# Kernel tuning notes

Hardware: AMD Instinct MI355X
Metric: run time of the kernel (lower is better)

The kernel has to match this reference:

```python
import jax, jax.numpy as jnp
import numpy as np

N_NODES = 100000
N_EDGES = 600000
NUM_GRAPHS = 512
IN_DIM = 128
HID = 64
HEADS = 2
NEG_SLOPE = 0.2


def gat_layer(h_in, src, dst, W, a_s, a_d, b, n_nodes):
    # W: [F_in, H*C], a_s/a_d: [H, C], b: [H*C]
    H, C = a_s.shape
    h = (h_in @ W).reshape(n_nodes, H, C)            # [N,H,C]
    alpha_src = jnp.einsum('nhc,hc->nh', h, a_s)      # [N,H]
    alpha_dst = jnp.einsum('nhc,hc->nh', h, a_d)      # [N,H]
    e = alpha_src[src] + alpha_dst[dst]               # [E,H]
    e = jnp.where(e >= 0, e, NEG_SLOPE * e)           # leaky_relu
    # segment softmax over destination node
    m = jax.ops.segment_max(e, dst, num_segments=n_nodes)
    m = jnp.where(jnp.isfinite(m), m, 0.0)
    ex = jnp.exp(e - m[dst])                          # [E,H]
    denom = jax.ops.segment_sum(ex, dst, num_segments=n_nodes)
    alpha = ex / jnp.maximum(denom[dst], 1e-16)       # [E,H]
    out = jax.ops.segment_sum(alpha[:, :, None] * h[src], dst, num_segments=n_nodes)
    return out.reshape(n_nodes, H * C) + b


def setup_inputs() -> dict:
    key = jax.random.key(0)
    ks = jax.random.split(key, 16)
    x = jax.random.normal(ks[0], (N_NODES, IN_DIM), dtype=jnp.float32)
    edge_index = jax.random.randint(ks[1], (2, N_EDGES), 0, N_NODES, dtype=jnp.int32)
    batch = jnp.sort(jax.random.randint(ks[2], (N_NODES,), 0, NUM_GRAPHS, dtype=jnp.int32))
    s = lambda *d: 1.0 / np.sqrt(d[0])
    W1 = jax.random.normal(ks[3], (IN_DIM, HEADS * HID), jnp.float32) * s(IN_DIM)
    a_src1 = jax.random.normal(ks[4], (HEADS, HID), jnp.float32) * s(HID)
    a_dst1 = jax.random.normal(ks[5], (HEADS, HID), jnp.float32) * s(HID)
    b1 = jnp.zeros((HEADS * HID,), jnp.float32)
    W2 = jax.random.normal(ks[6], (HEADS * HID, HID), jnp.float32) * s(HEADS * HID)
    a_src2 = jax.random.normal(ks[7], (1, HID), jnp.float32) * s(HID)
    a_dst2 = jax.random.normal(ks[8], (1, HID), jnp.float32) * s(HID)
    b2 = jnp.zeros((HID,), jnp.float32)
    Wf1 = jax.random.normal(ks[9], (2 * HID, HID), jnp.float32) * s(2 * HID)
    bf1 = jnp.zeros((HID,), jnp.float32)
    Wf2 = jax.random.normal(ks[10], (HID, 1), jnp.float32) * s(HID)
    bf2 = jnp.zeros((1,), jnp.float32)
    return dict(x=x, edge_index=edge_index, batch=batch, W1=W1, a_src1=a_src1,
                a_dst1=a_dst1, b1=b1, W2=W2, a_src2=a_src2, a_dst2=a_dst2, b2=b2,
                Wf1=Wf1, bf1=bf1, Wf2=Wf2, bf2=bf2)


def reference(x, edge_index, batch, W1, a_src1, a_dst1, b1, W2, a_src2, a_dst2, b2,
              Wf1, bf1, Wf2, bf2):
    n = x.shape[0]
    loops = jnp.arange(n, dtype=edge_index.dtype)
    src = jnp.concatenate([edge_index[0], loops])
    dst = jnp.concatenate([edge_index[1], loops])
    h = gat_layer(x, src, dst, W1, a_src1, a_dst1, b1, n)
    h = jax.nn.relu(h)
    h = gat_layer(h, src, dst, W2, a_src2, a_dst2, b2, n)  # [N, HID]
    # global mean + max pool per graph
    ones = jnp.ones((n,), h.dtype)
    counts = jax.ops.segment_sum(ones, batch, num_segments=NUM_GRAPHS)  # [G]
    mean = jax.ops.segment_sum(h, batch, num_segments=NUM_GRAPHS) / jnp.maximum(counts, 1.0)[:, None]
    mx = jax.ops.segment_max(h, batch, num_segments=NUM_GRAPHS)
    mx = jnp.where(counts[:, None] > 0, mx, 0.0)
    pooled = jnp.concatenate([mean, mx], axis=1)  # [G, 2*HID]
    out = jax.nn.relu(pooled @ Wf1 + bf1) @ Wf2 + bf2  # [G, 1]
    return out
```

## Files before the change

### kernel.cpp

```cpp
#include <hip/hip_runtime.h>

#define N_NODESC 100000
#define N_EDGESC 600000
#define E_TOTC   700000
#define NUM_GRAPHSC 512
#define NEG_SLOPE 0.2f
#define NEG_INF_ENC 0x007FFFFFu
#define SCAN_NB 128

typedef unsigned short ushort_t;
typedef __attribute__((ext_vector_type(8))) short bf16x8;
typedef __attribute__((ext_vector_type(4))) float f32x4;

__device__ __forceinline__ unsigned enc_f32(float f) {
    unsigned u = __float_as_uint(f);
    return (u & 0x80000000u) ? ~u : (u | 0x80000000u);
}
__device__ __forceinline__ float dec_f32(unsigned u) {
    u = (u & 0x80000000u) ? (u ^ 0x80000000u) : ~u;
    return __uint_as_float(u);
}
__device__ __forceinline__ ushort_t f32_to_bf16(float f) {
    unsigned u = __float_as_uint(f);
    return (ushort_t)((u + 0x7FFFu + ((u >> 16) & 1u)) >> 16);
}
__device__ __forceinline__ float bf16_to_f32(ushort_t h) {
    return __uint_as_float(((unsigned)h) << 16);
}
__device__ __forceinline__ unsigned pack_bf16x2(float a, float b) {
    return (unsigned)f32_to_bf16(a) | ((unsigned)f32_to_bf16(b) << 16);
}

__device__ __forceinline__ void glds16(const void* g, void* l) {
    __builtin_amdgcn_global_load_lds(
        (const __attribute__((address_space(1))) void*)g,
        (__attribute__((address_space(3))) void*)l, 16, 0, 0);
}

__global__ __launch_bounds__(256) void init_all(float* __restrict__ msum,
                                                unsigned* __restrict__ mmax,
                                                float* __restrict__ cnt,
                                                int* __restrict__ deg,
                                                const float* __restrict__ W1,
                                                const float* __restrict__ W2,
                                                ushort_t* __restrict__ wPre1,
                                                ushort_t* __restrict__ wPre2) {
    int i = blockIdx.x * 256 + threadIdx.x;
    if (i < NUM_GRAPHSC * 64) { msum[i] = 0.f; mmax[i] = NEG_INF_ENC; }
    if (i < NUM_GRAPHSC) cnt[i] = 0.f;
    if (i < N_NODESC) deg[i] = 0;
    if (i < 128 * 128) {
        int n = i >> 7, k = i & 127;
        wPre1[n * 128 + k] = f32_to_bf16(W1[k * 128 + n]);
    } else if (i < 128 * 128 + 64 * 128) {
        int j = i - 128 * 128;
        int n = j >> 7, k = j & 127;
        wPre2[n * 128 + k] = f32_to_bf16(W2[k * 64 + n]);
    }
}

__global__ __launch_bounds__(256) void hist_dst(const int* __restrict__ ei,
                                                int* __restrict__ deg) {
    int e = blockIdx.x * blockDim.x + threadIdx.x;
    if (e >= E_TOTC) return;
    int d = (e < N_EDGESC) ? ei[N_EDGESC + e] : e - N_EDGESC;
    atomicAdd(&deg[d], 1);
}

__global__ __launch_bounds__(256) void scan_partial(const int* __restrict__ deg,
                                                    int* __restrict__ bsum, int n) {
    __shared__ int red[256];
    int chunk = (n + SCAN_NB - 1) / SCAN_NB;
    int lo = blockIdx.x * chunk, hi = min(lo + chunk, n);
    int s = 0;
    for (int i = lo + threadIdx.x; i < hi; i += 256) s += deg[i];
    red[threadIdx.x] = s;
    __syncthreads();
    for (int d = 128; d; d >>= 1) {
        if (threadIdx.x < d) red[threadIdx.x] += red[threadIdx.x + d];
        __syncthreads();
    }
    if (threadIdx.x == 0) bsum[blockIdx.x] = red[0];
}

__global__ __launch_bounds__(256) void scan_final(const int* __restrict__ deg,
                                                  const int* __restrict__ bsum,
                                                  int* __restrict__ off, int n) {
    __shared__ int bs[SCAN_NB];
    __shared__ int tile[256];
    __shared__ int carry;
    int t = threadIdx.x;
    if (t < SCAN_NB) bs[t] = bsum[t];
    __syncthreads();
    for (int d = 1; d < SCAN_NB; d <<= 1) {
        int v = (t >= d && t < SCAN_NB) ? bs[t - d] : 0;
        __syncthreads();
        if (t < SCAN_NB) bs[t] += v;
        __syncthreads();
    }
    if (t == 0) carry = blockIdx.x ? bs[blockIdx.x - 1] : 0;
    __syncthreads();
    int chunk = (n + SCAN_NB - 1) / SCAN_NB;
    int lo = blockIdx.x * chunk, hi = min(lo + chunk, n);
    for (int base = lo; base < hi; base += 256) {
        int i = base + t;
        int v = (i < hi) ? deg[i] : 0;
        tile[t] = v;
        __syncthreads();
        for (int d = 1; d < 256; d <<= 1) {
            int u = (t >= d) ? tile[t - d] : 0;
            __syncthreads();
            tile[t] += u;
            __syncthreads();
        }
        if (i < hi) off[i] = carry + tile[t] - v;
        __syncthreads();
        if (t == 0) carry += tile[255];
        __syncthreads();
    }
}

__global__ __launch_bounds__(256) void scatter_csr(const int* __restrict__ ei,
                                                   int* __restrict__ off,
                                                   int* __restrict__ csr) {
    int e = blockIdx.x * blockDim.x + threadIdx.x;
    if (e >= E_TOTC) return;
    int s, d;
    if (e < N_EDGESC) { s = ei[e]; d = ei[N_EDGESC + e]; } else { s = d = e - N_EDGESC; }
    int slot = atomicAdd(&off[d], 1);
    csr[slot] = s;
}

__global__ __launch_bounds__(64) void gemm1_mfma(const float* __restrict__ X,
                                                 const ushort_t* __restrict__ Wp,
                                                 const float* __restrict__ a_s,
                                                 const float* __restrict__ a_d,
                                                 float* __restrict__ as_out,
                                                 float* __restrict__ ad_out,
                                                 ushort_t* __restrict__ Y16, int N) {
    __shared__ float sx[2048];
    int lane = threadIdx.x;
    int quad = lane >> 4, l16 = lane & 15;
    size_t node0 = (size_t)blockIdx.x * 16;

    {
        int rhalf = lane >> 5;
        int cb = (lane & 31) * 16;
#pragma unroll
        for (int c = 0; c < 8; ++c) {
            int rl = 2 * c + rhalf;
            size_t grow = node0 + rl;
            if (grow >= (size_t)N) grow = N - 1;
            int goff = cb ^ ((rl & 15) << 4);
            glds16((const char*)(X + grow * 128) + goff,
                   (char*)sx + c * 1024);
        }
    }
    asm volatile("s_waitcnt vmcnt(0)" ::: "memory");
    __builtin_amdgcn_sched_barrier(0);

    const char* swx = (const char*)sx + l16 * 512;
    int skey = (l16 & 15) << 4;

    f32x4 acc[8];
#pragma unroll
    for (int ct = 0; ct < 8; ++ct) acc[ct] = (f32x4){0.f, 0.f, 0.f, 0.f};

#pragma unroll
    for (int kc = 0; kc < 4; ++kc) {
        int b = kc * 128 + quad * 32;
        float4 xa = *(const float4*)(swx + (b ^ skey));
        float4 xb = *(const float4*)(swx + ((b + 16) ^ skey));
        union { bf16x8 v; unsigned u[4]; } af;
        af.u[0] = pack_bf16x2(xa.x, xa.y);
        af.u[1] = pack_bf16x2(xa.z, xa.w);
        af.u[2] = pack_bf16x2(xb.x, xb.y);
        af.u[3] = pack_bf16x2(xb.z, xb.w);
#pragma unroll
        for (int ct = 0; ct < 8; ++ct) {
            bf16x8 bb = *(const bf16x8*)(Wp + (size_t)(ct * 16 + l16) * 128 + kc * 32 + quad * 8);
            acc[ct] = __builtin_amdgcn_mfma_f32_16x16x32_bf16(af.v, bb, acc[ct], 0, 0, 0);
        }
    }

    unsigned* Yu = (unsigned*)Y16;
    float asv0[4], asv1[4], adv0[4], adv1[4];
#pragma unroll
    for (int ct = 0; ct < 4; ++ct) {
        int c = ct * 16 + l16;
        asv0[ct] = a_s[c]; asv1[ct] = a_s[64 + c];
        adv0[ct] = a_d[c]; adv1[ct] = a_d[64 + c];
    }
#pragma unroll
    for (int r = 0; r < 4; ++r) {
        size_t row = node0 + quad * 4 + r;
        bool ok = row < (size_t)N;
        if (ok) {
#pragma unroll
            for (int ct = 0; ct < 4; ++ct)
                Yu[row * 64 + ct * 16 + l16] = pack_bf16x2(acc[ct][r], acc[ct + 4][r]);
        }
        float ps0 = 0.f, pd0 = 0.f, ps1 = 0.f, pd1 = 0.f;
#pragma unroll
        for (int ct = 0; ct < 4; ++ct) {
            ps0 += acc[ct][r] * asv0[ct];     pd0 += acc[ct][r] * adv0[ct];
            ps1 += acc[ct + 4][r] * asv1[ct]; pd1 += acc[ct + 4][r] * adv1[ct];
        }
#pragma unroll
        for (int sh = 1; sh < 16; sh <<= 1) {
            ps0 += __shfl_xor(ps0, sh); pd0 += __shfl_xor(pd0, sh);
            ps1 += __shfl_xor(ps1, sh); pd1 += __shfl_xor(pd1, sh);
        }
        if (l16 == 0 && ok) {
            *(float2*)(as_out + row * 2) = make_float2(ps0, ps1);
            *(float2*)(ad_out + row * 2) = make_float2(pd0, pd1);
        }
    }
}

template <int H, bool RELU, bool FUSE2>
__global__ __launch_bounds__(256) void gat_gather(const int* __restrict__ off_end,
                                                  const int* __restrict__ deg,
                                                  const int* __restrict__ csr,
                                                  const float* __restrict__ as,
                                                  const float* __restrict__ ad,
                                                  const ushort_t* __restrict__ H16,
                                                  const float* __restrict__ b,
                                                  void* __restrict__ outp,
                                                  const ushort_t* __restrict__ Wp2,
                                                  const float* __restrict__ as2v,
                                                  const float* __restrict__ ad2v,
                                                  float* __restrict__ as2o,
                                                  float* __restrict__ ad2o,
                                                  ushort_t* __restrict__ h2out,
                                                  int N) {
    __shared__ char h1tile[16 * 256];
    __shared__ float aspart[16][4];
    __shared__ float adpart[16][4];
    int lane = threadIdx.x & 63;
    int wave = threadIdx.x >> 6;
    int l = lane & 15;
    int gbase = lane & 48;
    int n = blockIdx.x * 16 + wave * 4 + (lane >> 4);
    if (n >= N) return;
    int dg = deg[n];
    int o = off_end[n] - dg;
    float adv[H];
#pragma unroll
    for (int h = 0; h < H; ++h) adv[h] = ad[n * H + h];

    float acc[H][4], den[H];
#pragma unroll
    for (int h = 0; h < H; ++h) {
        den[h] = 0.f;
#pragma unroll
        for (int q = 0; q < 4; ++q) acc[h][q] = 0.f;
    }

    const unsigned* Hu = (const unsigned*)H16;

    for (int base = 0; base < dg; base += 16) {
        int i = base + l;
        bool valid = i < dg;
        int s = valid ? csr[o + i] : 0;
        float v[H];
        if (H == 2) {
            float2 p = valid ? ((const float2*)as)[s] : make_float2(0.f, 0.f);
            v[0] = p.x + adv[0];
            v[H - 1] = p.y + adv[H - 1];
        } else {
            v[0] = valid ? as[s] + adv[0] : 0.f;
        }
#pragma unroll
        for (int h = 0; h < H; ++h) {
            float e = v[h] >= 0.f ? v[h] : NEG_SLOPE * v[h];
            v[h] = valid ? __expf(e) : 0.f;
            den[h] += v[h];
        }
        int wpk = (H == 2) ? (int)pack_bf16x2(v[0], v[H - 1])
                           : (int)__float_as_uint(v[0]);
        int cnt = min(dg - base, 16);
        int cnt4 = (cnt + 3) & ~3;
        for (int j = 0; j < cnt4; j += 4) {
#pragma unroll
            for (int u = 0; u < 4; ++u) {
                int src = gbase + j + u;
                int sj = __shfl(s, src);
                int wp = __shfl(wpk, src);
                if (H == 2) {
                    float w0 = __uint_as_float(((unsigned)wp) << 16);
                    float w1 = __uint_as_float(((unsigned)wp) & 0xffff0000u);
                    uint4 hu = *(const uint4*)(Hu + (size_t)sj * 64 + l * 4);
                    acc[0][0] += w0 * __uint_as_float(hu.x << 16);
                    acc[H - 1][0] += w1 * __uint_as_float(hu.x & 0xffff0000u);
                    acc[0][1] += w0 * __uint_as_float(hu.y << 16);
                    acc[H - 1][1] += w1 * __uint_as_float(hu.y & 0xffff0000u);
                    acc[0][2] += w0 * __uint_as_float(hu.z << 16);
                    acc[H - 1][2] += w1 * __uint_as_float(hu.z & 0xffff0000u);
                    acc[0][3] += w0 * __uint_as_float(hu.w << 16);
                    acc[H - 1][3] += w1 * __uint_as_float(hu.w & 0xffff0000u);
                } else {
                    float w0 = __uint_as_float((unsigned)wp);
                    uint2 hu = *(const uint2*)((const unsigned*)(H16 + (size_t)sj * 64) + l * 2);
                    acc[0][0] += w0 * __uint_as_float(hu.x << 16);
                    acc[0][1] += w0 * __uint_as_float(hu.x & 0xffff0000u);
                    acc[0][2] += w0 * __uint_as_float(hu.y << 16);
                    acc[0][3] += w0 * __uint_as_float(hu.y & 0xffff0000u);
                }
            }
        }
    }
#pragma unroll
    for (int h = 0; h < H; ++h) {
#pragma unroll
        for (int sh = 8; sh; sh >>= 1) den[h] += __shfl_xor(den[h], sh);
    }
    if (H == 2) {
        float4 b0 = *(const float4*)(b + l * 4);
        float4 b1 = *(const float4*)(b + 64 + l * 4);
        float r0[4], r1[4];
        float id0 = 1.f / fmaxf(den[0], 1e-16f);
        float id1 = 1.f / fmaxf(den[H - 1], 1e-16f);
        r0[0] = acc[0][0] * id0 + b0.x; r0[1] = acc[0][1] * id0 + b0.y;
        r0[2] = acc[0][2] * id0 + b0.z; r0[3] = acc[0][3] * id0 + b0.w;
        r1[0] = acc[H - 1][0] * id1 + b1.x; r1[1] = acc[H - 1][1] * id1 + b1.y;
        r1[2] = acc[H - 1][2] * id1 + b1.z; r1[3] = acc[H - 1][3] * id1 + b1.w;
        if (RELU) {
#pragma unroll
            for (int q = 0; q < 4; ++q) { r0[q] = fmaxf(r0[q], 0.f); r1[q] = fmaxf(r1[q], 0.f); }
        }
        uint2 p0 = make_uint2(pack_bf16x2(r0[0], r0[1]), pack_bf16x2(r0[2], r0[3]));
        uint2 p1 = make_uint2(pack_bf16x2(r1[0], r1[1]), pack_bf16x2(r1[2], r1[3]));
        if (FUSE2) {
            int g = threadIdx.x >> 4;
            int key = (g & 15) << 4;
            *(uint2*)(h1tile + g * 256 + ((l * 8) ^ key)) = p0;
            *(uint2*)(h1tile + g * 256 + ((128 + l * 8) ^ key)) = p1;
        } else {
            ushort_t* outb = (ushort_t*)outp;
            *(uint2*)(outb + (size_t)n * 128 + l * 4) = p0;
            *(uint2*)(outb + (size_t)n * 128 + 64 + l * 4) = p1;
        }
    } else {
        float4 bv = *(const float4*)(b + l * 4);
        float id0 = 1.f / fmaxf(den[0], 1e-16f);
        float4 r;
        r.x = acc[0][0] * id0 + bv.x; r.y = acc[0][1] * id0 + bv.y;
        r.z = acc[0][2] * id0 + bv.z; r.w = acc[0][3] * id0 + bv.w;
        if (RELU) { r.x = fmaxf(r.x, 0.f); r.y = fmaxf(r.y, 0.f);
                    r.z = fmaxf(r.z, 0.f); r.w = fmaxf(r.w, 0.f); }
        *(float4*)((float*)outp + (size_t)n * 64 + l * 4) = r;
    }

    if (FUSE2) {
        __syncthreads();
        int quad = lane >> 4, l16 = lane & 15;
        int skey = (l16 & 15) << 4;
        const char* swx = h1tile + l16 * 256;
        f32x4 acc2 = (f32x4){0.f, 0.f, 0.f, 0.f};
#pragma unroll
        for (int kc = 0; kc < 4; ++kc) {
            int bb_ = kc * 64 + quad * 16;
            bf16x8 a = *(const bf16x8*)(swx + (bb_ ^ skey));
            bf16x8 bb = *(const bf16x8*)(Wp2 + (size_t)(wave * 16 + l16) * 128 + kc * 32 + quad * 8);
            acc2 = __builtin_amdgcn_mfma_f32_16x16x32_bf16(a, bb, acc2, 0, 0, 0);
        }
        float asv = as2v[wave * 16 + l16], adv2 = ad2v[wave * 16 + l16];
        size_t node0 = (size_t)blockIdx.x * 16;
#pragma unroll
        for (int r = 0; r < 4; ++r) {
            size_t row = node0 + quad * 4 + r;
            h2out[row * 64 + wave * 16 + l16] = f32_to_bf16(acc2[r]);
            float ps = acc2[r] * asv, pd = acc2[r] * adv2;
#pragma unroll
            for (int sh = 1; sh < 16; sh <<= 1) {
                ps += __shfl_xor(ps, sh);
                pd += __shfl_xor(pd, sh);
            }
            if (l16 == 0) {
                aspart[quad * 4 + r][wave] = ps;
                adpart[quad * 4 + r][wave] = pd;
            }
        }
        __syncthreads();
        int t = threadIdx.x;
        if (t < 16) {
            as2o[node0 + t] = aspart[t][0] + aspart[t][1] + aspart[t][2] + aspart[t][3];
        } else if (t < 32) {
            int rr = t - 16;
            ad2o[node0 + rr] = adpart[rr][0] + adpart[rr][1] + adpart[rr][2] + adpart[rr][3];
        }
    }
}

__global__ __launch_bounds__(256) void pool_nodes(const float* __restrict__ h2,
                                                  const int* __restrict__ batch,
                                                  float* __restrict__ msum,
                                                  unsigned* __restrict__ mmax,
                                                  float* __restrict__ cnt, int N) {
    int wid = threadIdx.x >> 6, lane = threadIdx.x & 63;
    int n0 = (blockIdx.x * 4 + wid) * 64;
    if (n0 >= N) return;
    int n1 = min(n0 + 64, N);
    int curg = batch[n0];
    float s = 0.f, m = -1e30f;
    int c = 0;
    for (int n = n0; n < n1; ++n) {
        int g = batch[n];
        float v = h2[(size_t)n * 64 + lane];
        if (g != curg) {
            atomicAdd(&msum[curg * 64 + lane], s);
            atomicMax(&mmax[curg * 64 + lane], enc_f32(m));
            if (lane == 0) atomicAdd(&cnt[curg], (float)c);
            s = 0.f; m = -1e30f; c = 0; curg = g;
        }
        s += v;
        m = fmaxf(m, v);
        ++c;
    }
    atomicAdd(&msum[curg * 64 + lane], s);
    atomicMax(&mmax[curg * 64 + lane], enc_f32(m));
    if (lane == 0) atomicAdd(&cnt[curg], (float)c);
}

__global__ __launch_bounds__(64) void mlp_head(const float* __restrict__ msum,
                                               const unsigned* __restrict__ mmax,
                                               const float* __restrict__ cnt,
                                               const float* __restrict__ Wf1,
                                               const float* __restrict__ bf1,
                                               const float* __restrict__ Wf2,
                                               const float* __restrict__ bf2,
                                               float* __restrict__ out) {
    __shared__ float pooled[128];
    int g = blockIdx.x, lane = threadIdx.x;
    float c = cnt[g];
    pooled[lane] = msum[g * 64 + lane] / fmaxf(c, 1.0f);
    pooled[64 + lane] = (c > 0.f) ? dec_f32(mmax[g * 64 + lane]) : 0.f;
    __syncthreads();
    float acc = bf1[lane];
#pragma unroll
    for (int k = 0; k < 128; ++k) acc += pooled[k] * Wf1[k * 64 + lane];
    acc = fmaxf(acc, 0.f);
    float r = acc * Wf2[lane];
#pragma unroll
    for (int off = 32; off; off >>= 1) r += __shfl_xor(r, off);
    if (lane == 0) out[g] = r + bf2[0];
}

extern "C" void kernel_launch(void* const* d_in, const int* in_sizes, int n_in,
                              void* d_out, int out_size, void* d_ws, size_t ws_size,
                              hipStream_t stream) {
    const float* x    = (const float*)d_in[0];
    const int*   ei   = (const int*)d_in[1];
    const int*   batch= (const int*)d_in[2];
    const float* W1   = (const float*)d_in[3];
    const float* as1  = (const float*)d_in[4];
    const float* ad1  = (const float*)d_in[5];
    const float* b1   = (const float*)d_in[6];
    const float* W2   = (const float*)d_in[7];
    const float* as2  = (const float*)d_in[8];
    const float* ad2  = (const float*)d_in[9];
    const float* b2   = (const float*)d_in[10];
    const float* Wf1  = (const float*)d_in[11];
    const float* bf1  = (const float*)d_in[12];
    const float* Wf2  = (const float*)d_in[13];
    const float* bf2  = (const float*)d_in[14];
    float* out = (float*)d_out;

    const size_t N = N_NODESC;
    float* ws = (float*)d_ws;
    ushort_t* h16_1 = (ushort_t*)ws;
    ushort_t* out1b = (ushort_t*)(ws + N * 64);
    ushort_t* h16_2 = (ushort_t*)(ws + N * 128);
    float*    out2  = ws + N * 160;
    float*    small = ws + N * 224;
    float*    as1b = small;
    float*    ad1b = small + 2 * N;
    float*    as2b = small + 4 * N;
    float*    ad2b = small + 5 * N;
    float*    msum = small + 6 * N;
    unsigned* mmax = (unsigned*)(small + 6 * N + 512 * 64);
    float*    cntb = small + 6 * N + 2 * 512 * 64;
    int* ip  = (int*)(small + 6 * N + 2 * 512 * 64 + 512);
    int* deg  = ip;
    int* off  = ip + N;
    int* csr  = ip + 2 * N;
    int* bsum = ip + 2 * N + E_TOTC;
    ushort_t* wPre1 = (ushort_t*)(bsum + SCAN_NB);
    ushort_t* wPre2 = wPre1 + 128 * 128;

    init_all<<<(N_NODESC + 255) / 256, 256, 0, stream>>>(msum, mmax, cntb, deg,
                                                         W1, W2, wPre1, wPre2);

    hist_dst<<<(E_TOTC + 255) / 256, 256, 0, stream>>>(ei, deg);
    scan_partial<<<SCAN_NB, 256, 0, stream>>>(deg, bsum, N);
    scan_final<<<SCAN_NB, 256, 0, stream>>>(deg, bsum, off, N);
    scatter_csr<<<(E_TOTC + 255) / 256, 256, 0, stream>>>(ei, off, csr);

    const int NBLK16 = (N_NODESC + 15) / 16;

    gemm1_mfma<<<NBLK16, 64, 0, stream>>>(x, wPre1, as1, ad1, as1b, ad1b, h16_1, N);
    gat_gather<2, true, true><<<NBLK16, 256, 0, stream>>>(
        off, deg, csr, as1b, ad1b, h16_1, b1, out1b,
        wPre2, as2, ad2, as2b, ad2b, h16_2, N);

    gat_gather<1, false, false><<<NBLK16, 256, 0, stream>>>(
        off, deg, csr, as2b, ad2b, h16_2, b2, out2,
        nullptr, nullptr, nullptr, nullptr, nullptr, nullptr, N);

    pool_nodes<<<(N + 255) / 256, 256, 0, stream>>>(out2, batch, msum, mmax, cntb, N);
    mlp_head<<<NUM_GRAPHSC, 64, 0, stream>>>(msum, mmax, cntb, Wf1, bf1, Wf2, bf2, out);
}
```

Measured before the change: 293.4 us.

## Stage neighbor feature rows into LDS via direct global-to-LDS loads in GAT gather

The gather loop now processes neighbors in batches of 8 instead of 16. Each wave copies the bf16 feature rows of those neighbors straight from global memory into a per-wave LDS buffer with 16-byte direct-to-LDS loads, waits for all of them, then runs the weighted accumulation from LDS. The aim is to issue every neighbor-row load up front and hide gather latency, instead of interleaving dependent global loads with the FMAs. In exchange the kernel gains a large per-block LDS buffer, which can lower occupancy. It also adds a full vmcnt wait every batch and doubles the number of loop iterations for high-degree nodes.

```diff
diff --git a/kernel.cpp b/kernel.cpp
--- a/kernel.cpp
+++ b/kernel.cpp
@@ -234,14 +234,16 @@
                                                   float* __restrict__ ad2o,
                                                   ushort_t* __restrict__ h2out,
                                                   int N) {
+    __shared__ char rbuf[4][(H == 2) ? 8192 : 4096];
     __shared__ char h1tile[16 * 256];
     __shared__ float aspart[16][4];
     __shared__ float adpart[16][4];
     int lane = threadIdx.x & 63;
     int wave = threadIdx.x >> 6;
     int l = lane & 15;
+    int g = lane >> 4;
     int gbase = lane & 48;
-    int n = blockIdx.x * 16 + wave * 4 + (lane >> 4);
+    int n = blockIdx.x * 16 + wave * 4 + g;
     if (n >= N) return;
     int dg = deg[n];
     int o = off_end[n] - dg;
@@ -257,11 +259,9 @@
         for (int q = 0; q < 4; ++q) acc[h][q] = 0.f;
     }
 
-    const unsigned* Hu = (const unsigned*)H16;
-
-    for (int base = 0; base < dg; base += 16) {
+    for (int base = 0; base < dg; base += 8) {
         int i = base + l;
-        bool valid = i < dg;
+        bool valid = (l < 8) && (i < dg);
         int s = valid ? csr[o + i] : 0;
         float v[H];
         if (H == 2) {
@@ -279,18 +279,37 @@
         }
         int wpk = (H == 2) ? (int)pack_bf16x2(v[0], v[H - 1])
                            : (int)__float_as_uint(v[0]);
-        int cnt = min(dg - base, 16);
-        int cnt4 = (cnt + 3) & ~3;
-        for (int j = 0; j < cnt4; j += 4) {
+
+        asm volatile("s_waitcnt lgkmcnt(0)" ::: "memory");
+        if (H == 2) {
+#pragma unroll
+            for (int c = 0; c < 8; ++c) {
+                int sjc = __shfl(s, gbase + c);
+                glds16((const char*)H16 + (size_t)(unsigned)sjc * 256 + l * 16,
+                       &rbuf[wave][c * 1024]);
+            }
+        } else {
+#pragma unroll
+            for (int k = 0; k < 4; ++k) {
+                int sjc = __shfl(s, gbase + 2 * k + (l >> 3));
+                glds16((const char*)H16 + (size_t)(unsigned)sjc * 128 + (l & 7) * 16,
+                       &rbuf[wave][k * 1024]);
+            }
+        }
+        asm volatile("s_waitcnt vmcnt(0)" ::: "memory");
+        __builtin_amdgcn_sched_barrier(0);
+
+        int cnt = min(dg - base, 8);
+        int cntR = (cnt + 3) & ~3;
+        for (int j = 0; j < cntR; j += 4) {
 #pragma unroll
             for (int u = 0; u < 4; ++u) {
-                int src = gbase + j + u;
-                int sj = __shfl(s, src);
-                int wp = __shfl(wpk, src);
+                int sl = j + u;
+                int wp = __shfl(wpk, gbase + sl);
                 if (H == 2) {
                     float w0 = __uint_as_float(((unsigned)wp) << 16);
                     float w1 = __uint_as_float(((unsigned)wp) & 0xffff0000u);
-                    uint4 hu = *(const uint4*)(Hu + (size_t)sj * 64 + l * 4);
+                    uint4 hu = *(const uint4*)&rbuf[wave][sl * 1024 + g * 256 + l * 16];
                     acc[0][0] += w0 * __uint_as_float(hu.x << 16);
                     acc[H - 1][0] += w1 * __uint_as_float(hu.x & 0xffff0000u);
                     acc[0][1] += w0 * __uint_as_float(hu.y << 16);
@@ -301,7 +320,7 @@
                     acc[H - 1][3] += w1 * __uint_as_float(hu.w & 0xffff0000u);
                 } else {
                     float w0 = __uint_as_float((unsigned)wp);
-                    uint2 hu = *(const uint2*)((const unsigned*)(H16 + (size_t)sj * 64) + l * 2);
+                    uint2 hu = *(const uint2*)&rbuf[wave][(sl >> 1) * 1024 + g * 256 + (sl & 1) * 128 + l * 8];
                     acc[0][0] += w0 * __uint_as_float(hu.x << 16);
                     acc[0][1] += w0 * __uint_as_float(hu.x & 0xffff0000u);
                     acc[0][2] += w0 * __uint_as_float(hu.y << 16);
@@ -332,10 +351,10 @@
         uint2 p0 = make_uint2(pack_bf16x2(r0[0], r0[1]), pack_bf16x2(r0[2], r0[3]));
         uint2 p1 = make_uint2(pack_bf16x2(r1[0], r1[1]), pack_bf16x2(r1[2], r1[3]));
         if (FUSE2) {
-            int g = threadIdx.x >> 4;
-            int key = (g & 15) << 4;
-            *(uint2*)(h1tile + g * 256 + ((l * 8) ^ key)) = p0;
-            *(uint2*)(h1tile + g * 256 + ((128 + l * 8) ^ key)) = p1;
+            int gg = threadIdx.x >> 4;
+            int key = (gg & 15) << 4;
+            *(uint2*)(h1tile + gg * 256 + ((l * 8) ^ key)) = p0;
+            *(uint2*)(h1tile + gg * 256 + ((128 + l * 8) ^ key)) = p1;
         } else {
             ushort_t* outb = (ushort_t*)outp;
             *(uint2*)(outb + (size_t)n * 128 + l * 4) = p0;
```

Result: slower. 311.3 us (+6.1%).

## Fuse graph mean/max pooling into second GAT gather kernel

Applied to the files above, without the earlier changes.

The second-layer gather now stages each block's 16 output rows in shared memory. It then performs the per-graph sum/max/count pooling with atomics directly, instead of writing the full node feature matrix to global memory. This removes the separate pool_nodes kernel, its launch, and a round trip of the N×64 float intermediate through memory. In exchange, atomic traffic rises because pooling segments are now 16 nodes per block instead of 64 per wave, and several blocks contend on the same graph accumulators.

```diff
diff --git a/kernel.cpp b/kernel.cpp
--- a/kernel.cpp
+++ b/kernel.cpp
@@ -218,7 +218,7 @@
     }
 }
 
-template <int H, bool RELU, bool FUSE2>
+template <int H, bool RELU, bool FUSE2, bool FPOOL>
 __global__ __launch_bounds__(256) void gat_gather(const int* __restrict__ off_end,
                                                   const int* __restrict__ deg,
                                                   const int* __restrict__ csr,
@@ -233,10 +233,15 @@
                                                   float* __restrict__ as2o,
                                                   float* __restrict__ ad2o,
                                                   ushort_t* __restrict__ h2out,
+                                                  const int* __restrict__ batchp,
+                                                  float* __restrict__ msum,
+                                                  unsigned* __restrict__ mmax,
+                                                  float* __restrict__ cntb,
                                                   int N) {
     __shared__ char h1tile[16 * 256];
     __shared__ float aspart[16][4];
     __shared__ float adpart[16][4];
+    __shared__ int batch_l[16];
     int lane = threadIdx.x & 63;
     int wave = threadIdx.x >> 6;
     int l = lane & 15;
@@ -349,7 +354,42 @@
         r.z = acc[0][2] * id0 + bv.z; r.w = acc[0][3] * id0 + bv.w;
         if (RELU) { r.x = fmaxf(r.x, 0.f); r.y = fmaxf(r.y, 0.f);
                     r.z = fmaxf(r.z, 0.f); r.w = fmaxf(r.w, 0.f); }
-        *(float4*)((float*)outp + (size_t)n * 64 + l * 4) = r;
+        if (FPOOL) {
+            float* pt = (float*)h1tile;
+            int gl = threadIdx.x >> 4;
+            *(float4*)(pt + gl * 64 + l * 4) = r;
+        } else {
+            *(float4*)((float*)outp + (size_t)n * 64 + l * 4) = r;
+        }
+    }
+
+    if (FPOOL) {
+        if (threadIdx.x < 16) batch_l[threadIdx.x] = batchp[blockIdx.x * 16 + threadIdx.x];
+        __syncthreads();
+        if (threadIdx.x < 64) {
+            int c = threadIdx.x;
+            const float* pt = (const float*)h1tile;
+            int curg = batch_l[0];
+            float s = 0.f, m = -1e30f;
+            int cc = 0;
+#pragma unroll
+            for (int i = 0; i < 16; ++i) {
+                int gg = batch_l[i];
+                float v = pt[i * 64 + c];
+                if (gg != curg) {
+                    atomicAdd(&msum[curg * 64 + c], s);
+                    atomicMax(&mmax[curg * 64 + c], enc_f32(m));
+                    if (c == 0) atomicAdd(&cntb[curg], (float)cc);
+                    s = 0.f; m = -1e30f; cc = 0; curg = gg;
+                }
+                s += v;
+                m = fmaxf(m, v);
+                ++cc;
+            }
+            atomicAdd(&msum[curg * 64 + c], s);
+            atomicMax(&mmax[curg * 64 + c], enc_f32(m));
+            if (c == 0) atomicAdd(&cntb[curg], (float)cc);
+        }
     }
 
     if (FUSE2) {
@@ -391,36 +431,6 @@
             ad2o[node0 + rr] = adpart[rr][0] + adpart[rr][1] + adpart[rr][2] + adpart[rr][3];
         }
     }
-}
-
-__global__ __launch_bounds__(256) void pool_nodes(const float* __restrict__ h2,
-                                                  const int* __restrict__ batch,
-                                                  float* __restrict__ msum,
-                                                  unsigned* __restrict__ mmax,
-                                                  float* __restrict__ cnt, int N) {
-    int wid = threadIdx.x >> 6, lane = threadIdx.x & 63;
-    int n0 = (blockIdx.x * 4 + wid) * 64;
-    if (n0 >= N) return;
-    int n1 = min(n0 + 64, N);
-    int curg = batch[n0];
-    float s = 0.f, m = -1e30f;
-    int c = 0;
-    for (int n = n0; n < n1; ++n) {
-        int g = batch[n];
-        float v = h2[(size_t)n * 64 + lane];
-        if (g != curg) {
-            atomicAdd(&msum[curg * 64 + lane], s);
-            atomicMax(&mmax[curg * 64 + lane], enc_f32(m));
-            if (lane == 0) atomicAdd(&cnt[curg], (float)c);
-            s = 0.f; m = -1e30f; c = 0; curg = g;
-        }
-        s += v;
-        m = fmaxf(m, v);
-        ++c;
-    }
-    atomicAdd(&msum[curg * 64 + lane], s);
-    atomicMax(&mmax[curg * 64 + lane], enc_f32(m));
-    if (lane == 0) atomicAdd(&cnt[curg], (float)c);
 }
 
 __global__ __launch_bounds__(64) void mlp_head(const float* __restrict__ msum,
@@ -488,6 +498,7 @@
     int* bsum = ip + 2 * N + E_TOTC;
     ushort_t* wPre1 = (ushort_t*)(bsum + SCAN_NB);
     ushort_t* wPre2 = wPre1 + 128 * 128;
+    (void)out1b; (void)out2;
 
     init_all<<<(N_NODESC + 255) / 256, 256, 0, stream>>>(msum, mmax, cntb, deg,
                                                          W1, W2, wPre1, wPre2);
@@ -500,14 +511,15 @@
     const int NBLK16 = (N_NODESC + 15) / 16;
 
     gemm1_mfma<<<NBLK16, 64, 0, stream>>>(x, wPre1, as1, ad1, as1b, ad1b, h16_1, N);
-    gat_gather<2, true, true><<<NBLK16, 256, 0, stream>>>(
-        off, deg, csr, as1b, ad1b, h16_1, b1, out1b,
-        wPre2, as2, ad2, as2b, ad2b, h16_2, N);
-
-    gat_gather<1, false, false><<<NBLK16, 256, 0, stream>>>(
-        off, deg, csr, as2b, ad2b, h16_2, b2, out2,
-        nullptr, nullptr, nullptr, nullptr, nullptr, nullptr, N);
-
-    pool_nodes<<<(N + 255) / 256, 256, 0, stream>>>(out2, batch, msum, mmax, cntb, N);
+    gat_gather<2, true, true, false><<<NBLK16, 256, 0, stream>>>(
+        off, deg, csr, as1b, ad1b, h16_1, b1, nullptr,
+        wPre2, as2, ad2, as2b, ad2b, h16_2,
+        nullptr, nullptr, nullptr, nullptr, N);
+
+    gat_gather<1, false, false, true><<<NBLK16, 256, 0, stream>>>(
+        off, deg, csr, as2b, ad2b, h16_2, b2, nullptr,
+        nullptr, nullptr, nullptr, nullptr, nullptr, nullptr,
+        batch, msum, mmax, cntb, N);
+
     mlp_head<<<NUM_GRAPHSC, 64, 0, stream>>>(msum, mmax, cntb, Wf1, bf1, Wf2, bf2, out);
 }
```

Measured after the change: 285.9 us. 1.03x faster.
